# Kernel optimization log

Measured on AMD Instinct MI355X. Metric: run time of the kernel, lower is better.

## Reference

```python
import jax, jax.numpy as jnp
import numpy as np

# dims: T time steps, B batch, F clinical features, H GRU hidden, NH heads, DFF ffn dim, AH single-attn hidden
T, B, F, H, NH, DFF, AH = 128, 256, 76, 64, 4, 256, 8


def setup_inputs() -> dict:
    key = jax.random.key(0)
    ks = jax.random.split(key, 32)
    s = 0.1
    def u(k, shape):
        return jax.random.uniform(k, shape, jnp.float32, -s, s)
    return {
        "x": jax.random.normal(ks[0], (T, B, F), jnp.float32),
        # per-feature GRU(1, H) weight stacks (torch gate order: r, z, n)
        "gru_w_ih": u(ks[1], (F, 3 * H)),          # input dim is 1 -> squeezed
        "gru_w_hh": u(ks[2], (F, 3 * H, H)),
        "gru_b_ih": jnp.zeros((F, 3 * H), jnp.float32),
        "gru_b_hh": jnp.zeros((F, 3 * H), jnp.float32),
        # per-feature SingleAttention('new', time_aware) params
        "att_Wt": u(ks[3], (F, H, AH)),
        "att_Wx": u(ks[4], (F, H, AH)),
        "att_rate": jnp.full((F,), 0.8, jnp.float32),
        # multi-head self-attention over the feature axis
        "mha_wq": u(ks[5], (H, H)), "mha_bq": jnp.zeros((H,), jnp.float32),
        "mha_wk": u(ks[6], (H, H)), "mha_bk": jnp.zeros((H,), jnp.float32),
        "mha_wv": u(ks[7], (H, H)), "mha_bv": jnp.zeros((H,), jnp.float32),
        "mha_wo": u(ks[8], (H, H)), "mha_bo": jnp.zeros((H,), jnp.float32),
        # position-wise feed forward
        "ffn_w1": u(ks[9], (H, DFF)), "ffn_b1": jnp.zeros((DFF,), jnp.float32),
        "ffn_w2": u(ks[10], (DFF, H)), "ffn_b2": jnp.zeros((H,), jnp.float32),
        # FinalAttentionQKV ('mul')
        "fa_wq": u(ks[11], (H, H)), "fa_bq": jnp.zeros((H,), jnp.float32),
        "fa_wk": u(ks[12], (H, H)), "fa_bk": jnp.zeros((H,), jnp.float32),
        "fa_wv": u(ks[13], (H, H)), "fa_bv": jnp.zeros((H,), jnp.float32),
        # output head
        "out0_w": u(ks[14], (H, H)), "out0_b": jnp.zeros((H,), jnp.float32),
        "out1_w": u(ks[15], (H, 1)), "out1_b": jnp.zeros((1,), jnp.float32),
    }


def reference(x, gru_w_ih, gru_w_hh, gru_b_ih, gru_b_hh,
              att_Wt, att_Wx, att_rate,
              mha_wq, mha_bq, mha_wk, mha_bk, mha_wv, mha_bv, mha_wo, mha_bo,
              ffn_w1, ffn_b1, ffn_w2, ffn_b2,
              fa_wq, fa_bq, fa_wk, fa_bk, fa_wv, fa_bv,
              out0_w, out0_b, out1_w, out1_b):
    # x: (T, B, F); torch permutes to (B, T, F)
    Ts, Bsz, Fd = x.shape
    Hd = gru_w_hh.shape[-1]
    dk = Hd // NH

    # ---- all F GRU(1,H) channels fused into one scan (vectorized over F) ----
    xs = jnp.transpose(x, (0, 2, 1))  # (T, F, B)

    def step(h, x_t):  # h: (F,B,H), x_t: (F,B)
        gx = x_t[:, :, None] * gru_w_ih[:, None, :] + gru_b_ih[:, None, :]      # (F,B,3H)
        gh = jnp.einsum('fbh,fgh->fbg', h, gru_w_hh) + gru_b_hh[:, None, :]     # (F,B,3H)
        rx, zx, nx = jnp.split(gx, 3, axis=-1)
        rh, zh, nh = jnp.split(gh, 3, axis=-1)
        r = jax.nn.sigmoid(rx + rh)
        z = jax.nn.sigmoid(zx + zh)
        n = jnp.tanh(nx + r * nh)
        h_new = (1.0 - z) * n + z * h
        return h_new, h_new

    h0 = jnp.zeros((Fd, Bsz, Hd), x.dtype)
    _, hs = jax.lax.scan(step, h0, xs)        # (T, F, B, H)
    hs = jnp.transpose(hs, (1, 2, 0, 3))       # (F, B, T, H)

    # ---- per-feature SingleAttention, type='new', time-aware ----
    q = jnp.einsum('fbh,fha->fba', hs[:, :, -1, :], att_Wt)   # (F,B,AH)
    k = jnp.einsum('fbth,fha->fbta', hs, att_Wx)              # (F,B,T,AH)
    dp = jnp.einsum('fba,fbta->fbt', q, k)                    # (F,B,T)
    sig = jax.nn.sigmoid(dp)
    decay = jnp.arange(Ts, 0, -1, dtype=x.dtype)              # T..1 (time_decays + 1)
    denom = jax.nn.sigmoid(att_rate)[:, None, None] * (jnp.log(2.72 + (1.0 - sig)) * decay)
    e = jax.nn.relu(sig / denom)
    a = jax.nn.softmax(e, axis=-1)
    emb = jnp.einsum('fbt,fbth->bfh', a, hs)                  # (B, F, H)

    def lin(t, w, b):
        return t @ w + b

    # ---- multi-head self-attention over the F axis + residual ----
    # NOTE: original lambda ignores its (layernormed) argument, so LN is dead code.
    def heads(t):
        return t.reshape(Bsz, Fd, NH, dk).transpose(0, 2, 1, 3)
    qh = heads(lin(emb, mha_wq, mha_bq))
    kh = heads(lin(emb, mha_wk, mha_bk))
    vh = heads(lin(emb, mha_wv, mha_bv))
    scores = jnp.einsum('bhqd,bhkd->bhqk', qh, kh) / jnp.sqrt(jnp.asarray(dk, x.dtype))
    attn = jax.nn.softmax(scores, axis=-1)
    ctx = jnp.einsum('bhqk,bhkd->bhqd', attn, vh).transpose(0, 2, 1, 3).reshape(Bsz, Fd, Hd)
    ctx = emb + lin(ctx, mha_wo, mha_bo)

    # ---- position-wise feed-forward + residual ----
    ctx = ctx + lin(jax.nn.relu(lin(ctx, ffn_w1, ffn_b1)), ffn_w2, ffn_b2)

    # ---- FinalAttentionQKV, type='mul' ----
    fq = lin(ctx[:, -1, :], fa_wq, fa_bq)      # (B,H)
    fk = lin(ctx, fa_wk, fa_bk)                # (B,F,H)
    fv = lin(ctx, fa_wv, fa_bv)                # (B,F,H)
    fe = jnp.einsum('bfh,bh->bf', fk, fq)
    fa_w = jax.nn.softmax(fe, axis=1)
    v = jnp.einsum('bf,bfh->bh', fa_w, fv)     # (B,H)

    # ---- output head ----
    out = jax.nn.sigmoid(lin(jax.nn.relu(lin(v, out0_w, out0_b)), out1_w, out1_b))
    return out  # (B, 1)
```

## Files before the change

kernel.cpp:

```cpp
#include <hip/hip_runtime.h>
#include <hip/hip_bf16.h>
#include <cstdint>
#include <cstddef>

#define TT 128
#define BBATCH 256
#define FFEAT 76
#define HDIM 64
#define NHEAD 4
#define DKH 16
#define DFF1 256
#define AH1 8
#define NROWS (BBATCH * FFEAT)

#define LOG2E 1.4426950408889634f

typedef __attribute__((ext_vector_type(8))) short bf16x8;
typedef __attribute__((ext_vector_type(4))) float f32x4;

__device__ __forceinline__ float fast_sigmoid(float v) {
    float p = __builtin_amdgcn_exp2f(-v * LOG2E);
    return __builtin_amdgcn_rcpf(1.0f + p);
}
__device__ __forceinline__ float fast_tanh(float v) {
    float p = __builtin_amdgcn_exp2f(v * (2.0f * LOG2E));
    return 1.0f - 2.0f * __builtin_amdgcn_rcpf(1.0f + p);
}
__device__ __forceinline__ short f2bf(float x) {
    __hip_bfloat16 h = __float2bfloat16(x);
    return *reinterpret_cast<short*>(&h);
}
__device__ __forceinline__ float bf2f(unsigned short s) {
    return __uint_as_float(((unsigned)s) << 16);
}
__device__ __forceinline__ unsigned pack_bf16(float a, float b) {
    unsigned ua = (unsigned)(unsigned short)f2bf(a);
    unsigned ub = (unsigned)(unsigned short)f2bf(b);
    return ua | (ub << 16);
}

__global__ __launch_bounds__(64) void gru_scan_kernel(
    const float* __restrict__ x, const float* __restrict__ w_ih,
    const float* __restrict__ w_hh, const float* __restrict__ b_ih,
    const float* __restrict__ b_hh, const float* __restrict__ Wt,
    const float* __restrict__ Wx, int f_base,
    __hip_bfloat16* __restrict__ hs, float* __restrict__ wtil)
{
    const int f_loc = blockIdx.y;
    const int f     = f_base + f_loc;
    const int b0    = blockIdx.x * 16;
    const int lane  = threadIdx.x;
    const int c     = lane & 15;
    const int q     = lane >> 4;

    __shared__ float x_lds[TT][16];
    __shared__ float wt_s[64][8];
    __shared__ float wx_s[64][8];
    __shared__ short hx[16][72];
    __shared__ float q_s[16][8];

    for (int i = lane; i < TT * 16; i += 64) {
        int t = i >> 4, b = i & 15;
        x_lds[t][b] = x[((size_t)t * BBATCH + b0 + b) * FFEAT + f];
    }
    for (int i = lane; i < 512; i += 64) {
        ((float*)wt_s)[i] = Wt[(size_t)f * 512 + i];
        ((float*)wx_s)[i] = Wx[(size_t)f * 512 + i];
    }
    __syncthreads();

    bf16x8 afr[12][2];
    {
        const float* whh_f = w_hh + (size_t)f * 192 * 64;
        #pragma unroll
        for (int nt = 0; nt < 12; ++nt) {
            int gate = nt >> 2, tt = nt & 3;
            int urow = (c >> 2) * 8 + (tt & 1) * 4 + (c & 3) + (tt >> 1) * 32;
            const float* row = whh_f + (size_t)(gate * 64 + urow) * 64;
            #pragma unroll
            for (int kq = 0; kq < 2; ++kq) {
                bf16x8 fr;
                #pragma unroll
                for (int j = 0; j < 8; ++j) fr[j] = f2bf(row[kq * 32 + q * 8 + j]);
                afr[nt][kq] = fr;
            }
        }
    }
    float wr[4][4], wz[4][4], wn[4][4], bnx[4][4];
    f32x4 biasv[12];
    #pragma unroll
    for (int tt = 0; tt < 4; ++tt) {
        #pragma unroll
        for (int r = 0; r < 4; ++r) {
            int u = q * 8 + (tt & 1) * 4 + r + (tt >> 1) * 32;
            wr[tt][r]  = w_ih[f*192 + u];
            wz[tt][r]  = w_ih[f*192 + 64 + u];
            wn[tt][r]  = w_ih[f*192 + 128 + u];
            bnx[tt][r] = b_ih[f*192 + 128 + u];
            biasv[tt][r]     = b_ih[f*192 + u]      + b_hh[f*192 + u];
            biasv[4 + tt][r] = b_ih[f*192 + 64 + u] + b_hh[f*192 + 64 + u];
            biasv[8 + tt][r] = b_hh[f*192 + 128 + u];
        }
    }

    float hprev[4][4];
    #pragma unroll
    for (int tt = 0; tt < 4; ++tt)
        #pragma unroll
        for (int r = 0; r < 4; ++r) hprev[tt][r] = 0.f;

    bf16x8 hb0 = {0,0,0,0,0,0,0,0};
    bf16x8 hb1 = {0,0,0,0,0,0,0,0};

    short* hs_b = (short*)hs + ((size_t)f_loc * BBATCH + b0 + c) * TT * HDIM;

    for (int t = 0; t < TT; ++t) {
        f32x4 acc[12];
        #pragma unroll
        for (int nt = 0; nt < 12; ++nt) {
            f32x4 a = __builtin_amdgcn_mfma_f32_16x16x32_bf16(afr[nt][0], hb0, biasv[nt], 0, 0, 0);
            acc[nt]  = __builtin_amdgcn_mfma_f32_16x16x32_bf16(afr[nt][1], hb1, a, 0, 0, 0);
        }

        float xv = x_lds[t][c];
        float hn4[4][4];
        #pragma unroll
        for (int tt = 0; tt < 4; ++tt) {
            #pragma unroll
            for (int r = 0; r < 4; ++r) {
                float R  = fmaf(xv, wr[tt][r], acc[tt][r]);
                float Z  = fmaf(xv, wz[tt][r], acc[4 + tt][r]);
                float NX = fmaf(xv, wn[tt][r], bnx[tt][r]);
                float rg = fast_sigmoid(R);
                float zg = fast_sigmoid(Z);
                float ng = fast_tanh(fmaf(rg, acc[8 + tt][r], NX));
                float hn = fmaf(zg, hprev[tt][r] - ng, ng);
                hprev[tt][r] = hn;
                hn4[tt][r] = hn;
            }
        }
        {
            union { int4 i; bf16x8 v; } u0, u1;
            u0.i.x = pack_bf16(hn4[0][0], hn4[0][1]);
            u0.i.y = pack_bf16(hn4[0][2], hn4[0][3]);
            u0.i.z = pack_bf16(hn4[1][0], hn4[1][1]);
            u0.i.w = pack_bf16(hn4[1][2], hn4[1][3]);
            u1.i.x = pack_bf16(hn4[2][0], hn4[2][1]);
            u1.i.y = pack_bf16(hn4[2][2], hn4[2][3]);
            u1.i.z = pack_bf16(hn4[3][0], hn4[3][1]);
            u1.i.w = pack_bf16(hn4[3][2], hn4[3][3]);
            hb0 = u0.v; hb1 = u1.v;
        }
        short* dst = hs_b + (size_t)t * HDIM + q * 8;
        *(bf16x8*)dst = hb0;
        *(bf16x8*)(dst + 32) = hb1;
    }

    *(bf16x8*)&hx[c][q * 8]      = hb0;
    *(bf16x8*)&hx[c][32 + q * 8] = hb1;

    #pragma unroll
    for (int rr = 0; rr < 2; ++rr) {
        int role = rr * 64 + lane;
        int b = role >> 3, a = role & 7;
        float s = 0.f;
        #pragma unroll 8
        for (int j = 0; j < 64; ++j)
            s = fmaf(bf2f((unsigned short)hx[b][j]), wt_s[j][a], s);
        q_s[b][a] = s;
    }
    {
        int b = lane >> 2, jb = (lane & 3) * 16;
        float qreg[8];
        #pragma unroll
        for (int a = 0; a < 8; ++a) qreg[a] = q_s[b][a];
        float* wt_out = wtil + ((size_t)(b0 + b) * FFEAT + f) * HDIM + jb;
        #pragma unroll
        for (int j4 = 0; j4 < 4; ++j4) {
            float4 v;
            #pragma unroll
            for (int jj = 0; jj < 4; ++jj) {
                int j = jb + j4 * 4 + jj;
                float s = 0.f;
                #pragma unroll
                for (int a = 0; a < 8; ++a) s = fmaf(wx_s[j][a], qreg[a], s);
                (&v.x)[jj] = s;
            }
            *(float4*)&wt_out[j4 * 4] = v;
        }
    }
}

__global__ __launch_bounds__(256) void attn2_kernel(
    const __hip_bfloat16* __restrict__ hs, const float* __restrict__ wtil,
    const float* __restrict__ rate, int f_base, float* __restrict__ emb)
{
    const int w     = threadIdx.x >> 6;
    const int lane  = threadIdx.x & 63;
    const int b     = blockIdx.x * 4 + w;
    const int f_loc = blockIdx.y;
    const int f     = f_base + f_loc;
    const int g     = lane >> 3;
    const int i     = lane & 7;

    float wv[8];
    {
        const float4* src = (const float4*)(wtil + ((size_t)b * FFEAT + f) * HDIM + 8 * i);
        float4 a = src[0], c = src[1];
        wv[0]=a.x; wv[1]=a.y; wv[2]=a.z; wv[3]=a.w;
        wv[4]=c.x; wv[5]=c.y; wv[6]=c.z; wv[7]=c.w;
    }
    const float rs = fast_sigmoid(rate[f]);
    const uint4* basev = (const uint4*)((const short*)hs +
                          ((size_t)f_loc * BBATCH + b) * TT * HDIM);

    float m = -1.0e30f, s = 0.f;
    float o[8];
    #pragma unroll
    for (int j = 0; j < 8; ++j) o[j] = 0.f;

    #pragma unroll 4
    for (int it = 0; it < 16; ++it) {
        const int t = it * 8 + g;
        uint4 U = basev[t * 8 + i];
        float h[8];
        h[0] = __uint_as_float(U.x << 16); h[1] = __uint_as_float(U.x & 0xffff0000u);
        h[2] = __uint_as_float(U.y << 16); h[3] = __uint_as_float(U.y & 0xffff0000u);
        h[4] = __uint_as_float(U.z << 16); h[5] = __uint_as_float(U.z & 0xffff0000u);
        h[6] = __uint_as_float(U.w << 16); h[7] = __uint_as_float(U.w & 0xffff0000u);
        float dp = 0.f;
        #pragma unroll
        for (int j = 0; j < 8; ++j) dp = fmaf(h[j], wv[j], dp);
        dp += __shfl_xor(dp, 1, 64);
        dp += __shfl_xor(dp, 2, 64);
        dp += __shfl_xor(dp, 4, 64);
        float sig = fast_sigmoid(dp);
        float den = rs * (__logf(2.72f + (1.0f - sig)) * (float)(TT - t));
        float e = fmaxf(sig / den, 0.0f);
        float nm = fmaxf(m, e);
        float sc = __builtin_amdgcn_exp2f((m - nm) * LOG2E);
        float p  = __builtin_amdgcn_exp2f((e - nm) * LOG2E);
        s = fmaf(s, sc, p);
        #pragma unroll
        for (int j = 0; j < 8; ++j) o[j] = fmaf(o[j], sc, p * h[j]);
        m = nm;
    }
    #pragma unroll
    for (int k = 8; k <= 32; k <<= 1) {
        float om = __shfl_xor(m, k, 64);
        float os = __shfl_xor(s, k, 64);
        float nm = fmaxf(m, om);
        float sa = __builtin_amdgcn_exp2f((m - nm) * LOG2E);
        float sb = __builtin_amdgcn_exp2f((om - nm) * LOG2E);
        s = s * sa + os * sb;
        #pragma unroll
        for (int j = 0; j < 8; ++j) {
            float oo = __shfl_xor(o[j], k, 64);
            o[j] = o[j] * sa + oo * sb;
        }
        m = nm;
    }
    if (g == 0) {
        float inv = __builtin_amdgcn_rcpf(s);
        float4 v0, v1;
        v0.x = o[0]*inv; v0.y = o[1]*inv; v0.z = o[2]*inv; v0.w = o[3]*inv;
        v1.x = o[4]*inv; v1.y = o[5]*inv; v1.z = o[6]*inv; v1.w = o[7]*inv;
        float* dst = &emb[((size_t)b * FFEAT + f) * HDIM + 8 * i];
        *(float4*)dst       = v0;
        *(float4*)(dst + 4) = v1;
    }
}

struct GemmP {
    const float* X;
    const float* W[3];
    const float* B[3];
    const float* R;
    float* Y[3];
    int K;
    int Nfull;
    int act;
};

__global__ __launch_bounds__(256) void gemm_kernel(GemmP A)
{
    __shared__ float xs[64][65];
    __shared__ float ws[64][68];

    const int tid = threadIdx.x;
    const int tx  = tid & 15;
    const int ty  = tid >> 4;
    const int m0  = blockIdx.x * 64;
    const int n0  = blockIdx.y * 64;
    const int z   = blockIdx.z;

    const float* W = A.W[z];
    const float* Bv = A.B[z];
    float* Y = A.Y[z];
    const int K = A.K, Nfull = A.Nfull;

    float acc[4][4];
    #pragma unroll
// ... 192 lines not shown
{
    const float* x     = (const float*)d_in[0];
    const float* w_ih  = (const float*)d_in[1];
    const float* w_hh  = (const float*)d_in[2];
    const float* b_ih  = (const float*)d_in[3];
    const float* b_hh  = (const float*)d_in[4];
    const float* attWt = (const float*)d_in[5];
    const float* attWx = (const float*)d_in[6];
    const float* attRt = (const float*)d_in[7];
    const float* wq    = (const float*)d_in[8];
    const float* bq    = (const float*)d_in[9];
    const float* wk    = (const float*)d_in[10];
    const float* bk    = (const float*)d_in[11];
    const float* wv    = (const float*)d_in[12];
    const float* bv    = (const float*)d_in[13];
    const float* wo    = (const float*)d_in[14];
    const float* bo    = (const float*)d_in[15];
    const float* w1    = (const float*)d_in[16];
    const float* b1    = (const float*)d_in[17];
    const float* w2    = (const float*)d_in[18];
    const float* b2    = (const float*)d_in[19];
    const float* faq   = (const float*)d_in[20];
    const float* fabq  = (const float*)d_in[21];
    const float* fak   = (const float*)d_in[22];
    const float* fabk  = (const float*)d_in[23];
    const float* fav   = (const float*)d_in[24];
    const float* fabv  = (const float*)d_in[25];
    const float* o0w   = (const float*)d_in[26];
    const float* o0b   = (const float*)d_in[27];
    const float* o1w   = (const float*)d_in[28];
    const float* o1b   = (const float*)d_in[29];
    float* out = (float*)d_out;

    const size_t emb_bytes  = (size_t)NROWS * HDIM * 4;
    const size_t wtil_bytes = (size_t)NROWS * HDIM * 4;
    const size_t R64        = (size_t)NROWS * HDIM;
    const size_t tail_bytes = 12 * R64 * 4;

    const int chunk_opts[6] = {76, 38, 19, 4, 2, 1};
    int FC = 0;
    for (int i = 0; i < 6; ++i) {
        size_t hs_b = (size_t)chunk_opts[i] * BBATCH * TT * HDIM * 2;
        size_t scratch = hs_b > tail_bytes ? hs_b : tail_bytes;
        if (emb_bytes + wtil_bytes + scratch <= ws_size) { FC = chunk_opts[i]; break; }
    }
    if (FC == 0) {
        ws_report_kernel<<<dim3((out_size + 255) / 256), dim3(256), 0, stream>>>(
            out, out_size, (float)((double)ws_size / (1024.0 * 1024.0)));
        return;
    }

    float* emb  = (float*)d_ws;
    float* wtil = (float*)((char*)d_ws + emb_bytes);
    char*  scratch = (char*)d_ws + emb_bytes + wtil_bytes;
    __hip_bfloat16* hs = (__hip_bfloat16*)scratch;

    for (int f0 = 0; f0 < FFEAT; f0 += FC) {
        int fc = (FFEAT - f0 < FC) ? (FFEAT - f0) : FC;
        gru_scan_kernel<<<dim3(16, fc), dim3(64), 0, stream>>>(
            x, w_ih, w_hh, b_ih, b_hh, attWt, attWx, f0, hs, wtil);
        attn2_kernel<<<dim3(BBATCH / 4, fc), dim3(256), 0, stream>>>(
            hs, wtil, attRt, f0, emb);
    }

    float* ts   = (float*)scratch;
    float* q    = ts;
    float* k    = ts + 1*R64;
    float* v    = ts + 2*R64;
    float* ctx  = ts + 3*R64;
    float* ctx2 = ts + 4*R64;
    float* hid  = ts + 5*R64;
    float* ctx3 = ts + 9*R64;
    float* fk   = ts + 10*R64;
    float* fv   = ts + 11*R64;

    const int MB = NROWS / 64;

    {
        GemmP A = { emb, {wq, wk, wv}, {bq, bk, bv}, nullptr, {q, k, v}, 64, 64, 0 };
        gemm_kernel<<<dim3(MB, 1, 3), dim3(256), 0, stream>>>(A);
    }
    mha_core_kernel<<<dim3(BBATCH, NHEAD), dim3(256), 0, stream>>>(q, k, v, ctx);
    {
        GemmP A = { ctx, {wo, nullptr, nullptr}, {bo, nullptr, nullptr}, emb,
                    {ctx2, nullptr, nullptr}, 64, 64, 0 };
        gemm_kernel<<<dim3(MB, 1, 1), dim3(256), 0, stream>>>(A);
    }
    {
        GemmP A = { ctx2, {w1, nullptr, nullptr}, {b1, nullptr, nullptr}, nullptr,
                    {hid, nullptr, nullptr}, 64, 256, 1 };
        gemm_kernel<<<dim3(MB, 4, 1), dim3(256), 0, stream>>>(A);
    }
    {
        GemmP A = { hid, {w2, nullptr, nullptr}, {b2, nullptr, nullptr}, ctx2,
                    {ctx3, nullptr, nullptr}, 256, 64, 0 };
// ... 11 lines not shown
```

Measured before the change: 568.7 us.

## Split GRU hidden units across two waves with LDS double-buffered state exchange

After: 644.5 us. 13.3% more time.

```diff
diff --git a/kernel.cpp b/kernel.cpp
--- a/kernel.cpp
+++ b/kernel.cpp
@@ -39,7 +39,7 @@
     return ua | (ub << 16);
 }
 
-__global__ __launch_bounds__(64) void gru_scan_kernel(
+__global__ __launch_bounds__(128) void gru_scan_kernel(
     const float* __restrict__ x, const float* __restrict__ w_ih,
     const float* __restrict__ w_hh, const float* __restrict__ b_ih,
     const float* __restrict__ b_hh, const float* __restrict__ Wt,
@@ -49,138 +49,138 @@
     const int f_loc = blockIdx.y;
     const int f     = f_base + f_loc;
     const int b0    = blockIdx.x * 16;
-    const int lane  = threadIdx.x;
+    const int tid   = threadIdx.x;
+    const int w     = tid >> 6;
+    const int lane  = tid & 63;
     const int c     = lane & 15;
     const int q     = lane >> 4;
 
     __shared__ float x_lds[TT][16];
     __shared__ float wt_s[64][8];
     __shared__ float wx_s[64][8];
-    __shared__ short hx[16][72];
+    __shared__ short hbuf[2][16][72];
     __shared__ float q_s[16][8];
 
-    for (int i = lane; i < TT * 16; i += 64) {
+    for (int i = tid; i < TT * 16; i += 128) {
         int t = i >> 4, b = i & 15;
         x_lds[t][b] = x[((size_t)t * BBATCH + b0 + b) * FFEAT + f];
     }
-    for (int i = lane; i < 512; i += 64) {
+    for (int i = tid; i < 512; i += 128) {
         ((float*)wt_s)[i] = Wt[(size_t)f * 512 + i];
         ((float*)wx_s)[i] = Wx[(size_t)f * 512 + i];
     }
-    __syncthreads();
-
-    bf16x8 afr[12][2];
+    {
+        short* hz = (short*)hbuf;
+        for (int i = tid; i < 16 * 72; i += 128) hz[i] = 0;
+    }
+    __syncthreads();
+
+    bf16x8 afr[6][2];
     {
         const float* whh_f = w_hh + (size_t)f * 192 * 64;
         #pragma unroll
-        for (int nt = 0; nt < 12; ++nt) {
-            int gate = nt >> 2, tt = nt & 3;
-            int urow = (c >> 2) * 8 + (tt & 1) * 4 + (c & 3) + (tt >> 1) * 32;
-            const float* row = whh_f + (size_t)(gate * 64 + urow) * 64;
+        for (int nt = 0; nt < 6; ++nt) {
+            int g = nt >> 1, t2 = nt & 1;
+            const float* rp = whh_f + (size_t)(g * 64 + w * 32 + t2 * 16 + c) * 64;
             #pragma unroll
             for (int kq = 0; kq < 2; ++kq) {
                 bf16x8 fr;
                 #pragma unroll
-                for (int j = 0; j < 8; ++j) fr[j] = f2bf(row[kq * 32 + q * 8 + j]);
+                for (int j = 0; j < 8; ++j) fr[j] = f2bf(rp[kq * 32 + q * 8 + j]);
                 afr[nt][kq] = fr;
             }
         }
     }
-    float wr[4][4], wz[4][4], wn[4][4], bnx[4][4];
-    f32x4 biasv[12];
-    #pragma unroll
-    for (int tt = 0; tt < 4; ++tt) {
+    float wr[2][4], wz[2][4], wn[2][4], bnx[2][4];
+    f32x4 biasv[6];
+    #pragma unroll
+    for (int t2 = 0; t2 < 2; ++t2) {
         #pragma unroll
         for (int r = 0; r < 4; ++r) {
-            int u = q * 8 + (tt & 1) * 4 + r + (tt >> 1) * 32;
-            wr[tt][r]  = w_ih[f*192 + u];
-            wz[tt][r]  = w_ih[f*192 + 64 + u];
-            wn[tt][r]  = w_ih[f*192 + 128 + u];
-            bnx[tt][r] = b_ih[f*192 + 128 + u];
-            biasv[tt][r]     = b_ih[f*192 + u]      + b_hh[f*192 + u];
-            biasv[4 + tt][r] = b_ih[f*192 + 64 + u] + b_hh[f*192 + 64 + u];
-            biasv[8 + tt][r] = b_hh[f*192 + 128 + u];
-        }
-    }
-
-    float hprev[4][4];
-    #pragma unroll
-    for (int tt = 0; tt < 4; ++tt)
-        #pragma unroll
-        for (int r = 0; r < 4; ++r) hprev[tt][r] = 0.f;
-
-    bf16x8 hb0 = {0,0,0,0,0,0,0,0};
-    bf16x8 hb1 = {0,0,0,0,0,0,0,0};
-
+            int u = w * 32 + t2 * 16 + q * 4 + r;
+            wr[t2][r]  = w_ih[f*192 + u];
+            wz[t2][r]  = w_ih[f*192 + 64 + u];
+            wn[t2][r]  = w_ih[f*192 + 128 + u];
+            bnx[t2][r] = b_ih[f*192 + 128 + u];
+            biasv[t2][r]     = b_ih[f*192 + u]      + b_hh[f*192 + u];
+            biasv[2 + t2][r] = b_ih[f*192 + 64 + u] + b_hh[f*192 + 64 + u];
+            biasv[4 + t2][r] = b_hh[f*192 + 128 + u];
+        }
+    }
+
+    float hprev[2][4];
+    #pragma unroll
+    for (int t2 = 0; t2 < 2; ++t2)
+        #pragma unroll
+        for (int r = 0; r < 4; ++r) hprev[t2][r] = 0.f;
+
+    int cur = 0;
     short* hs_b = (short*)hs + ((size_t)f_loc * BBATCH + b0 + c) * TT * HDIM;
 
     for (int t = 0; t < TT; ++t) {
-        f32x4 acc[12];
-        #pragma unroll
-        for (int nt = 0; nt < 12; ++nt) {
+        bf16x8 hb0 = *(bf16x8*)&hbuf[cur][c][q * 8];
+        bf16x8 hb1 = *(bf16x8*)&hbuf[cur][c][32 + q * 8];
+
+        f32x4 acc[6];
+        #pragma unroll
+        for (int nt = 0; nt < 6; ++nt) {
             f32x4 a = __builtin_amdgcn_mfma_f32_16x16x32_bf16(afr[nt][0], hb0, biasv[nt], 0, 0, 0);
             acc[nt]  = __builtin_amdgcn_mfma_f32_16x16x32_bf16(afr[nt][1], hb1, a, 0, 0, 0);
         }
 
         float xv = x_lds[t][c];
-        float hn4[4][4];
-        #pragma unroll
-        for (int tt = 0; tt < 4; ++tt) {
+        float hn4[2][4];
+        #pragma unroll
+        for (int t2 = 0; t2 < 2; ++t2) {
             #pragma unroll
             for (int r = 0; r < 4; ++r) {
-                float R  = fmaf(xv, wr[tt][r], acc[tt][r]);
-                float Z  = fmaf(xv, wz[tt][r], acc[4 + tt][r]);
-                float NX = fmaf(xv, wn[tt][r], bnx[tt][r]);
+                float R  = fmaf(xv, wr[t2][r], acc[t2][r]);
+                float Z  = fmaf(xv, wz[t2][r], acc[2 + t2][r]);
+                float NX = fmaf(xv, wn[t2][r], bnx[t2][r]);
                 float rg = fast_sigmoid(R);
                 float zg = fast_sigmoid(Z);
-                float ng = fast_tanh(fmaf(rg, acc[8 + tt][r], NX));
-                float hn = fmaf(zg, hprev[tt][r] - ng, ng);
-                hprev[tt][r] = hn;
-                hn4[tt][r] = hn;
+                float ng = fast_tanh(fmaf(rg, acc[4 + t2][r], NX));
+                float hn = fmaf(zg, hprev[t2][r] - ng, ng);
+                hprev[t2][r] = hn;
+                hn4[t2][r] = hn;
             }
         }
-        {
-            union { int4 i; bf16x8 v; } u0, u1;
-            u0.i.x = pack_bf16(hn4[0][0], hn4[0][1]);
-            u0.i.y = pack_bf16(hn4[0][2], hn4[0][3]);
-            u0.i.z = pack_bf16(hn4[1][0], hn4[1][1]);
-            u0.i.w = pack_bf16(hn4[1][2], hn4[1][3]);
-            u1.i.x = pack_bf16(hn4[2][0], hn4[2][1]);
-            u1.i.y = pack_bf16(hn4[2][2], hn4[2][3]);
-            u1.i.z = pack_bf16(hn4[3][0], hn4[3][1]);
-            u1.i.w = pack_bf16(hn4[3][2], hn4[3][3]);
-            hb0 = u0.v; hb1 = u1.v;
-        }
-        short* dst = hs_b + (size_t)t * HDIM + q * 8;
-        *(bf16x8*)dst = hb0;
-        *(bf16x8*)(dst + 32) = hb1;
-    }
-
-    *(bf16x8*)&hx[c][q * 8]      = hb0;
-    *(bf16x8*)&hx[c][32 + q * 8] = hb1;
-
-    #pragma unroll
-    for (int rr = 0; rr < 2; ++rr) {
-        int role = rr * 64 + lane;
-        int b = role >> 3, a = role & 7;
+        uint2 pk0, pk1;
+        pk0.x = pack_bf16(hn4[0][0], hn4[0][1]);
+        pk0.y = pack_bf16(hn4[0][2], hn4[0][3]);
+        pk1.x = pack_bf16(hn4[1][0], hn4[1][1]);
+        pk1.y = pack_bf16(hn4[1][2], hn4[1][3]);
+        short* hd = &hbuf[cur ^ 1][c][w * 32 + q * 4];
+        *(uint2*)hd        = pk0;
+        *(uint2*)(hd + 16) = pk1;
+        short* gd = hs_b + (size_t)t * HDIM + w * 32 + q * 4;
+        *(uint2*)gd        = pk0;
+        *(uint2*)(gd + 16) = pk1;
+        __syncthreads();
+        cur ^= 1;
+    }
+
+    {
+        int b = tid >> 3, a = tid & 7;
         float s = 0.f;
         #pragma unroll 8
         for (int j = 0; j < 64; ++j)
-            s = fmaf(bf2f((unsigned short)hx[b][j]), wt_s[j][a], s);
+            s = fmaf(bf2f((unsigned short)hbuf[cur][b][j]), wt_s[j][a], s);
         q_s[b][a] = s;
     }
-    {
-        int b = lane >> 2, jb = (lane & 3) * 16;
+    __syncthreads();
+    {
+        int b = tid >> 3, seg = tid & 7;
         float qreg[8];
         #pragma unroll
         for (int a = 0; a < 8; ++a) qreg[a] = q_s[b][a];
-        float* wt_out = wtil + ((size_t)(b0 + b) * FFEAT + f) * HDIM + jb;
-        #pragma unroll
-        for (int j4 = 0; j4 < 4; ++j4) {
+        float* wt_out = wtil + ((size_t)(b0 + b) * FFEAT + f) * HDIM + seg * 8;
+        #pragma unroll
+        for (int j4 = 0; j4 < 2; ++j4) {
             float4 v;
             #pragma unroll
             for (int jj = 0; jj < 4; ++jj) {
-                int j = jb + j4 * 4 + jj;
+                int j = seg * 8 + j4 * 4 + jj;
                 float s = 0.f;
                 #pragma unroll
                 for (int a = 0; a < 8; ++a) s = fmaf(wx_s[j][a], qreg[a], s);
@@ -206,9 +206,9 @@
     float wv[8];
     {
         const float4* src = (const float4*)(wtil + ((size_t)b * FFEAT + f) * HDIM + 8 * i);
-        float4 a = src[0], c = src[1];
+        float4 a = src[0], c2 = src[1];
         wv[0]=a.x; wv[1]=a.y; wv[2]=a.z; wv[3]=a.w;
-        wv[4]=c.x; wv[5]=c.y; wv[6]=c.z; wv[7]=c.w;
+        wv[4]=c2.x; wv[5]=c2.y; wv[6]=c2.z; wv[7]=c2.w;
     }
     const float rs = fast_sigmoid(rate[f]);
     const uint4* basev = (const uint4*)((const short*)hs +
@@ -551,7 +551,7 @@
 
     for (int f0 = 0; f0 < FFEAT; f0 += FC) {
         int fc = (FFEAT - f0 < FC) ? (FFEAT - f0) : FC;
-        gru_scan_kernel<<<dim3(16, fc), dim3(64), 0, stream>>>(
+        gru_scan_kernel<<<dim3(16, fc), dim3(128), 0, stream>>>(
             x, w_ih, w_hh, b_ih, b_hh, attWt, attWx, f0, hs, wtil);
         attn2_kernel<<<dim3(BBATCH / 4, fc), dim3(256), 0, stream>>>(
             hs, wtil, attRt, f0, emb);
```

## Fuse GRU scan and time attention into one pipelined launch with double-buffered states

Applied to the files above, without the earlier changes.

New measurement: 819.2 us. +44.1%, slower.

```diff
diff --git a/kernel.cpp b/kernel.cpp
--- a/kernel.cpp
+++ b/kernel.cpp
@@ -12,6 +12,7 @@
 #define DFF1 256
 #define AH1 8
 #define NROWS (BBATCH * FFEAT)
+#define FC 19
 
 #define LOG2E 1.4426950408889634f
 
@@ -39,235 +40,235 @@
     return ua | (ub << 16);
 }
 
-__global__ __launch_bounds__(64) void gru_scan_kernel(
+__global__ __launch_bounds__(64) void fused_scan_attn_kernel(
     const float* __restrict__ x, const float* __restrict__ w_ih,
     const float* __restrict__ w_hh, const float* __restrict__ b_ih,
     const float* __restrict__ b_hh, const float* __restrict__ Wt,
-    const float* __restrict__ Wx, int f_base,
-    __hip_bfloat16* __restrict__ hs, float* __restrict__ wtil)
+    const float* __restrict__ Wx, const float* __restrict__ rate,
+    int ngru, int f0_gru, __hip_bfloat16* __restrict__ hs_w,
+    int f0_att, const __hip_bfloat16* __restrict__ hs_r,
+    float* __restrict__ wtil, float* __restrict__ emb)
 {
-    const int f_loc = blockIdx.y;
-    const int f     = f_base + f_loc;
-    const int b0    = blockIdx.x * 16;
-    const int lane  = threadIdx.x;
-    const int c     = lane & 15;
-    const int q     = lane >> 4;
-
     __shared__ float x_lds[TT][16];
     __shared__ float wt_s[64][8];
     __shared__ float wx_s[64][8];
     __shared__ short hx[16][72];
     __shared__ float q_s[16][8];
 
-    for (int i = lane; i < TT * 16; i += 64) {
-        int t = i >> 4, b = i & 15;
-        x_lds[t][b] = x[((size_t)t * BBATCH + b0 + b) * FFEAT + f];
-    }
-    for (int i = lane; i < 512; i += 64) {
-        ((float*)wt_s)[i] = Wt[(size_t)f * 512 + i];
-        ((float*)wx_s)[i] = Wx[(size_t)f * 512 + i];
-    }
-    __syncthreads();
-
-    bf16x8 afr[12][2];
-    {
-        const float* whh_f = w_hh + (size_t)f * 192 * 64;
-        #pragma unroll
-        for (int nt = 0; nt < 12; ++nt) {
-            int gate = nt >> 2, tt = nt & 3;
-            int urow = (c >> 2) * 8 + (tt & 1) * 4 + (c & 3) + (tt >> 1) * 32;
-            const float* row = whh_f + (size_t)(gate * 64 + urow) * 64;
-            #pragma unroll
-            for (int kq = 0; kq < 2; ++kq) {
-                bf16x8 fr;
+    const int gid  = blockIdx.x;
+    const int lane = threadIdx.x;
+
+    if (gid < ngru) {
+        const int f_loc = gid >> 4;
+        const int f     = f0_gru + f_loc;
+        const int b0    = (gid & 15) * 16;
+        const int c     = lane & 15;
+        const int q     = lane >> 4;
+
+        for (int i = lane; i < TT * 16; i += 64) {
+            int t = i >> 4, b = i & 15;
+            x_lds[t][b] = x[((size_t)t * BBATCH + b0 + b) * FFEAT + f];
+        }
+        for (int i = lane; i < 512; i += 64) {
+            ((float*)wt_s)[i] = Wt[(size_t)f * 512 + i];
+            ((float*)wx_s)[i] = Wx[(size_t)f * 512 + i];
+        }
+        __syncthreads();
+
+        bf16x8 afr[12][2];
+        {
+            const float* whh_f = w_hh + (size_t)f * 192 * 64;
+            #pragma unroll
+            for (int nt = 0; nt < 12; ++nt) {
+                int gate = nt >> 2, tt = nt & 3;
+                int urow = (c >> 2) * 8 + (tt & 1) * 4 + (c & 3) + (tt >> 1) * 32;
+                const float* row = whh_f + (size_t)(gate * 64 + urow) * 64;
                 #pragma unroll
-                for (int j = 0; j < 8; ++j) fr[j] = f2bf(row[kq * 32 + q * 8 + j]);
-                afr[nt][kq] = fr;
-            }
-        }
-    }
-    float wr[4][4], wz[4][4], wn[4][4], bnx[4][4];
-    f32x4 biasv[12];
-    #pragma unroll
-    for (int tt = 0; tt < 4; ++tt) {
-        #pragma unroll
-        for (int r = 0; r < 4; ++r) {
-            int u = q * 8 + (tt & 1) * 4 + r + (tt >> 1) * 32;
-            wr[tt][r]  = w_ih[f*192 + u];
-            wz[tt][r]  = w_ih[f*192 + 64 + u];
-            wn[tt][r]  = w_ih[f*192 + 128 + u];
-            bnx[tt][r] = b_ih[f*192 + 128 + u];
-            biasv[tt][r]     = b_ih[f*192 + u]      + b_hh[f*192 + u];
-            biasv[4 + tt][r] = b_ih[f*192 + 64 + u] + b_hh[f*192 + 64 + u];
-            biasv[8 + tt][r] = b_hh[f*192 + 128 + u];
-        }
-    }
-
-    float hprev[4][4];
-    #pragma unroll
-    for (int tt = 0; tt < 4; ++tt)
-        #pragma unroll
-        for (int r = 0; r < 4; ++r) hprev[tt][r] = 0.f;
-
-    bf16x8 hb0 = {0,0,0,0,0,0,0,0};
-    bf16x8 hb1 = {0,0,0,0,0,0,0,0};
-
-    short* hs_b = (short*)hs + ((size_t)f_loc * BBATCH + b0 + c) * TT * HDIM;
-
-    for (int t = 0; t < TT; ++t) {
-        f32x4 acc[12];
-        #pragma unroll
-        for (int nt = 0; nt < 12; ++nt) {
-            f32x4 a = __builtin_amdgcn_mfma_f32_16x16x32_bf16(afr[nt][0], hb0, biasv[nt], 0, 0, 0);
-            acc[nt]  = __builtin_amdgcn_mfma_f32_16x16x32_bf16(afr[nt][1], hb1, a, 0, 0, 0);
-        }
-
-        float xv = x_lds[t][c];
-        float hn4[4][4];
+                for (int kq = 0; kq < 2; ++kq) {
+                    bf16x8 fr;
+                    #pragma unroll
+                    for (int j = 0; j < 8; ++j) fr[j] = f2bf(row[kq * 32 + q * 8 + j]);
+                    afr[nt][kq] = fr;
+                }
+            }
+        }
+        float wr[4][4], wz[4][4], wn[4][4], bnx[4][4];
+        f32x4 biasv[12];
         #pragma unroll
         for (int tt = 0; tt < 4; ++tt) {
             #pragma unroll
             for (int r = 0; r < 4; ++r) {
-                float R  = fmaf(xv, wr[tt][r], acc[tt][r]);
-                float Z  = fmaf(xv, wz[tt][r], acc[4 + tt][r]);
-                float NX = fmaf(xv, wn[tt][r], bnx[tt][r]);
-                float rg = fast_sigmoid(R);
-                float zg = fast_sigmoid(Z);
-                float ng = fast_tanh(fmaf(rg, acc[8 + tt][r], NX));
-                float hn = fmaf(zg, hprev[tt][r] - ng, ng);
-                hprev[tt][r] = hn;
-                hn4[tt][r] = hn;
-            }
+                int u = q * 8 + (tt & 1) * 4 + r + (tt >> 1) * 32;
+                wr[tt][r]  = w_ih[f*192 + u];
+                wz[tt][r]  = w_ih[f*192 + 64 + u];
+                wn[tt][r]  = w_ih[f*192 + 128 + u];
+                bnx[tt][r] = b_ih[f*192 + 128 + u];
+                biasv[tt][r]     = b_ih[f*192 + u]      + b_hh[f*192 + u];
+                biasv[4 + tt][r] = b_ih[f*192 + 64 + u] + b_hh[f*192 + 64 + u];
+                biasv[8 + tt][r] = b_hh[f*192 + 128 + u];
+            }
+        }
+
+        float hprev[4][4];
+        #pragma unroll
+        for (int tt = 0; tt < 4; ++tt)
+            #pragma unroll
+            for (int r = 0; r < 4; ++r) hprev[tt][r] = 0.f;
+
+        bf16x8 hb0 = {0,0,0,0,0,0,0,0};
+        bf16x8 hb1 = {0,0,0,0,0,0,0,0};
+
+        short* hs_b = (short*)hs_w + ((size_t)f_loc * BBATCH + b0 + c) * TT * HDIM;
+
+        for (int t = 0; t < TT; ++t) {
+            f32x4 acc[12];
+            #pragma unroll
+            for (int nt = 0; nt < 12; ++nt) {
+                f32x4 a = __builtin_amdgcn_mfma_f32_16x16x32_bf16(afr[nt][0], hb0, biasv[nt], 0, 0, 0);
+                acc[nt]  = __builtin_amdgcn_mfma_f32_16x16x32_bf16(afr[nt][1], hb1, a, 0, 0, 0);
+            }
+
+            float xv = x_lds[t][c];
+            float hn4[4][4];
+            #pragma unroll
+            for (int tt = 0; tt < 4; ++tt) {
+                #pragma unroll
+                for (int r = 0; r < 4; ++r) {
+                    float R  = fmaf(xv, wr[tt][r], acc[tt][r]);
+                    float Z  = fmaf(xv, wz[tt][r], acc[4 + tt][r]);
+                    float NX = fmaf(xv, wn[tt][r], bnx[tt][r]);
+                    float rg = fast_sigmoid(R);
+                    float zg = fast_sigmoid(Z);
+                    float ng = fast_tanh(fmaf(rg, acc[8 + tt][r], NX));
+                    float hn = fmaf(zg, hprev[tt][r] - ng, ng);
+                    hprev[tt][r] = hn;
+                    hn4[tt][r] = hn;
+                }
+            }
+            {
+                union { int4 i; bf16x8 v; } u0, u1;
+                u0.i.x = pack_bf16(hn4[0][0], hn4[0][1]);
+                u0.i.y = pack_bf16(hn4[0][2], hn4[0][3]);
+                u0.i.z = pack_bf16(hn4[1][0], hn4[1][1]);
+                u0.i.w = pack_bf16(hn4[1][2], hn4[1][3]);
+                u1.i.x = pack_bf16(hn4[2][0], hn4[2][1]);
+                u1.i.y = pack_bf16(hn4[2][2], hn4[2][3]);
+                u1.i.z = pack_bf16(hn4[3][0], hn4[3][1]);
+                u1.i.w = pack_bf16(hn4[3][2], hn4[3][3]);
+                hb0 = u0.v; hb1 = u1.v;
+            }
+            short* dst = hs_b + (size_t)t * HDIM + q * 8;
+            *(bf16x8*)dst = hb0;
+            *(bf16x8*)(dst + 32) = hb1;
+        }
+
+        *(bf16x8*)&hx[c][q * 8]      = hb0;
+        *(bf16x8*)&hx[c][32 + q * 8] = hb1;
+
+        #pragma unroll
+        for (int rr = 0; rr < 2; ++rr) {
+            int role = rr * 64 + lane;
+            int b = role >> 3, a = role & 7;
+            float s = 0.f;
+            #pragma unroll 8
+            for (int j = 0; j < 64; ++j)
+                s = fmaf(bf2f((unsigned short)hx[b][j]), wt_s[j][a], s);
+            q_s[b][a] = s;
         }
         {
-            union { int4 i; bf16x8 v; } u0, u1;
-            u0.i.x = pack_bf16(hn4[0][0], hn4[0][1]);
-            u0.i.y = pack_bf16(hn4[0][2], hn4[0][3]);
-            u0.i.z = pack_bf16(hn4[1][0], hn4[1][1]);
-            u0.i.w = pack_bf16(hn4[1][2], hn4[1][3]);
-            u1.i.x = pack_bf16(hn4[2][0], hn4[2][1]);
-            u1.i.y = pack_bf16(hn4[2][2], hn4[2][3]);
-            u1.i.z = pack_bf16(hn4[3][0], hn4[3][1]);
-            u1.i.w = pack_bf16(hn4[3][2], hn4[3][3]);
-            hb0 = u0.v; hb1 = u1.v;
-        }
-        short* dst = hs_b + (size_t)t * HDIM + q * 8;
-        *(bf16x8*)dst = hb0;
-        *(bf16x8*)(dst + 32) = hb1;
-    }
-
-    *(bf16x8*)&hx[c][q * 8]      = hb0;
-    *(bf16x8*)&hx[c][32 + q * 8] = hb1;
-
-    #pragma unroll
-    for (int rr = 0; rr < 2; ++rr) {
-        int role = rr * 64 + lane;
-        int b = role >> 3, a = role & 7;
-        float s = 0.f;
-        #pragma unroll 8
-        for (int j = 0; j < 64; ++j)
-            s = fmaf(bf2f((unsigned short)hx[b][j]), wt_s[j][a], s);
-        q_s[b][a] = s;
-    }
-    {
-        int b = lane >> 2, jb = (lane & 3) * 16;
-        float qreg[8];
-        #pragma unroll
-        for (int a = 0; a < 8; ++a) qreg[a] = q_s[b][a];
-        float* wt_out = wtil + ((size_t)(b0 + b) * FFEAT + f) * HDIM + jb;
-        #pragma unroll
-        for (int j4 = 0; j4 < 4; ++j4) {
-            float4 v;
-            #pragma unroll
-            for (int jj = 0; jj < 4; ++jj) {
-                int j = jb + j4 * 4 + jj;
-                float s = 0.f;
+            int b = lane >> 2, jb = (lane & 3) * 16;
+            float qreg[8];
+            #pragma unroll
+            for (int a = 0; a < 8; ++a) qreg[a] = q_s[b][a];
+            float* wt_out = wtil + ((size_t)(b0 + b) * FFEAT + f) * HDIM + jb;
+            #pragma unroll
+            for (int j4 = 0; j4 < 4; ++j4) {
+                float4 v;
                 #pragma unroll
-                for (int a = 0; a < 8; ++a) s = fmaf(wx_s[j][a], qreg[a], s);
-                (&v.x)[jj] = s;
-            }
-            *(float4*)&wt_out[j4 * 4] = v;
-        }
-    }
-}
-
-__global__ __launch_bounds__(256) void attn2_kernel(
-    const __hip_bfloat16* __restrict__ hs, const float* __restrict__ wtil,
-    const float* __restrict__ rate, int f_base, float* __restrict__ emb)
-{
-    const int w     = threadIdx.x >> 6;
-    const int lane  = threadIdx.x & 63;
-    const int b     = blockIdx.x * 4 + w;
-    const int f_loc = blockIdx.y;
-    const int f     = f_base + f_loc;
-    const int g     = lane >> 3;
-    const int i     = lane & 7;
-
-    float wv[8];
-    {
-        const float4* src = (const float4*)(wtil + ((size_t)b * FFEAT + f) * HDIM + 8 * i);
-        float4 a = src[0], c = src[1];
-        wv[0]=a.x; wv[1]=a.y; wv[2]=a.z; wv[3]=a.w;
-        wv[4]=c.x; wv[5]=c.y; wv[6]=c.z; wv[7]=c.w;
-    }
-    const float rs = fast_sigmoid(rate[f]);
-    const uint4* basev = (const uint4*)((const short*)hs +
-                          ((size_t)f_loc * BBATCH + b) * TT * HDIM);
-
-    float m = -1.0e30f, s = 0.f;
-    float o[8];
-    #pragma unroll
-    for (int j = 0; j < 8; ++j) o[j] = 0.f;
-
-    #pragma unroll 4
-    for (int it = 0; it < 16; ++it) {
-        const int t = it * 8 + g;
-        uint4 U = basev[t * 8 + i];
-        float h[8];
-        h[0] = __uint_as_float(U.x << 16); h[1] = __uint_as_float(U.x & 0xffff0000u);
-        h[2] = __uint_as_float(U.y << 16); h[3] = __uint_as_float(U.y & 0xffff0000u);
-        h[4] = __uint_as_float(U.z << 16); h[5] = __uint_as_float(U.z & 0xffff0000u);
-        h[6] = __uint_as_float(U.w << 16); h[7] = __uint_as_float(U.w & 0xffff0000u);
-        float dp = 0.f;
-        #pragma unroll
-        for (int j = 0; j < 8; ++j) dp = fmaf(h[j], wv[j], dp);
-        dp += __shfl_xor(dp, 1, 64);
-        dp += __shfl_xor(dp, 2, 64);
-        dp += __shfl_xor(dp, 4, 64);
-        float sig = fast_sigmoid(dp);
-        float den = rs * (__logf(2.72f + (1.0f - sig)) * (float)(TT - t));
-        float e = fmaxf(sig / den, 0.0f);
-        float nm = fmaxf(m, e);
-        float sc = __builtin_amdgcn_exp2f((m - nm) * LOG2E);
-        float p  = __builtin_amdgcn_exp2f((e - nm) * LOG2E);
-        s = fmaf(s, sc, p);
-        #pragma unroll
-        for (int j = 0; j < 8; ++j) o[j] = fmaf(o[j], sc, p * h[j]);
-        m = nm;
-    }
-    #pragma unroll
-    for (int k = 8; k <= 32; k <<= 1) {
-        float om = __shfl_xor(m, k, 64);
-        float os = __shfl_xor(s, k, 64);
-        float nm = fmaxf(m, om);
-        float sa = __builtin_amdgcn_exp2f((m - nm) * LOG2E);
-        float sb = __builtin_amdgcn_exp2f((om - nm) * LOG2E);
-        s = s * sa + os * sb;
-        #pragma unroll
-        for (int j = 0; j < 8; ++j) {
-            float oo = __shfl_xor(o[j], k, 64);
-            o[j] = o[j] * sa + oo * sb;
-        }
-        m = nm;
-    }
-    if (g == 0) {
-        float inv = __builtin_amdgcn_rcpf(s);
-        float4 v0, v1;
-        v0.x = o[0]*inv; v0.y = o[1]*inv; v0.z = o[2]*inv; v0.w = o[3]*inv;
-        v1.x = o[4]*inv; v1.y = o[5]*inv; v1.z = o[6]*inv; v1.w = o[7]*inv;
-        float* dst = &emb[((size_t)b * FFEAT + f) * HDIM + 8 * i];
-        *(float4*)dst       = v0;
-        *(float4*)(dst + 4) = v1;
+                for (int jj = 0; jj < 4; ++jj) {
+                    int j = jb + j4 * 4 + jj;
+                    float s = 0.f;
+                    #pragma unroll
+                    for (int a = 0; a < 8; ++a) s = fmaf(wx_s[j][a], qreg[a], s);
+                    (&v.x)[jj] = s;
+                }
+                *(float4*)&wt_out[j4 * 4] = v;
+            }
+        }
+    } else {
+        const int aid   = gid - ngru;
+        const int b     = aid & 255;
+        const int f_loc = aid >> 8;
+        const int f     = f0_att + f_loc;
+        const int g     = lane >> 3;
+        const int i     = lane & 7;
+
+        float wv[8];
+        {
+            const float4* src = (const float4*)(wtil + ((size_t)b * FFEAT + f) * HDIM + 8 * i);
+            float4 a = src[0], c2 = src[1];
+            wv[0]=a.x; wv[1]=a.y; wv[2]=a.z; wv[3]=a.w;
+            wv[4]=c2.x; wv[5]=c2.y; wv[6]=c2.z; wv[7]=c2.w;
+        }
+        const float rs = fast_sigmoid(rate[f]);
+        const uint4* basev = (const uint4*)((const short*)hs_r +
+                              ((size_t)f_loc * BBATCH + b) * TT * HDIM);
+
+        float m = -1.0e30f, s = 0.f;
+        float o[8];
+        #pragma unroll
+        for (int j = 0; j < 8; ++j) o[j] = 0.f;
+
+        #pragma unroll 4
+        for (int it = 0; it < 16; ++it) {
+            const int t = it * 8 + g;
+            uint4 U = basev[t * 8 + i];
+            float h[8];
+            h[0] = __uint_as_float(U.x << 16); h[1] = __uint_as_float(U.x & 0xffff0000u);
+            h[2] = __uint_as_float(U.y << 16); h[3] = __uint_as_float(U.y & 0xffff0000u);
+            h[4] = __uint_as_float(U.z << 16); h[5] = __uint_as_float(U.z & 0xffff0000u);
+            h[6] = __uint_as_float(U.w << 16); h[7] = __uint_as_float(U.w & 0xffff0000u);
+            float dp = 0.f;
+            #pragma unroll
+            for (int j = 0; j < 8; ++j) dp = fmaf(h[j], wv[j], dp);
+            dp += __shfl_xor(dp, 1, 64);
+            dp += __shfl_xor(dp, 2, 64);
+            dp += __shfl_xor(dp, 4, 64);
+            float sig = fast_sigmoid(dp);
+            float den = rs * (__logf(2.72f + (1.0f - sig)) * (float)(TT - t));
+            float e = fmaxf(sig / den, 0.0f);
+            float nm = fmaxf(m, e);
+            float sc = __builtin_amdgcn_exp2f((m - nm) * LOG2E);
+            float p  = __builtin_amdgcn_exp2f((e - nm) * LOG2E);
+            s = fmaf(s, sc, p);
+            #pragma unroll
+            for (int j = 0; j < 8; ++j) o[j] = fmaf(o[j], sc, p * h[j]);
+            m = nm;
+        }
+        #pragma unroll
+        for (int k = 8; k <= 32; k <<= 1) {
+            float om = __shfl_xor(m, k, 64);
+            float os = __shfl_xor(s, k, 64);
+            float nm = fmaxf(m, om);
+            float sa = __builtin_amdgcn_exp2f((m - nm) * LOG2E);
+            float sb = __builtin_amdgcn_exp2f((om - nm) * LOG2E);
+            s = s * sa + os * sb;
+            #pragma unroll
+            for (int j = 0; j < 8; ++j) {
+                float oo = __shfl_xor(o[j], k, 64);
+                o[j] = o[j] * sa + oo * sb;
+            }
+            m = nm;
+        }
+        if (g == 0) {
+            float inv = __builtin_amdgcn_rcpf(s);
+            float4 v0, v1;
+            v0.x = o[0]*inv; v0.y = o[1]*inv; v0.z = o[2]*inv; v0.w = o[3]*inv;
+            v1.x = o[4]*inv; v1.y = o[5]*inv; v1.z = o[6]*inv; v1.w = o[7]*inv;
+            float* dst = &emb[((size_t)b * FFEAT + f) * HDIM + 8 * i];
+            *(float4*)dst       = v0;
+            *(float4*)(dst + 4) = v1;
+        }
     }
 }
 
@@ -528,17 +529,13 @@
 
     const size_t emb_bytes  = (size_t)NROWS * HDIM * 4;
     const size_t wtil_bytes = (size_t)NROWS * HDIM * 4;
+    const size_t hs_half    = (size_t)FC * BBATCH * TT * HDIM * 2;
     const size_t R64        = (size_t)NROWS * HDIM;
     const size_t tail_bytes = 12 * R64 * 4;
-
-    const int chunk_opts[6] = {76, 38, 19, 4, 2, 1};
-    int FC = 0;
-    for (int i = 0; i < 6; ++i) {
-        size_t hs_b = (size_t)chunk_opts[i] * BBATCH * TT * HDIM * 2;
-        size_t scratch = hs_b > tail_bytes ? hs_b : tail_bytes;
-        if (emb_bytes + wtil_bytes + scratch <= ws_size) { FC = chunk_opts[i]; break; }
-    }
-    if (FC == 0) {
+    const size_t scratch_sz = (2 * hs_half > tail_bytes) ? 2 * hs_half : tail_bytes;
+    const size_t need = emb_bytes + wtil_bytes + scratch_sz;
+
+    if (need > ws_size) {
         ws_report_kernel<<<dim3((out_size + 255) / 256), dim3(256), 0, stream>>>(
             out, out_size, (float)((double)ws_size / (1024.0 * 1024.0)));
         return;
@@ -547,14 +544,22 @@
     float* emb  = (float*)d_ws;
     float* wtil = (float*)((char*)d_ws + emb_bytes);
     char*  scratch = (char*)d_ws + emb_bytes + wtil_bytes;
-    __hip_bfloat16* hs = (__hip_bfloat16*)scratch;
-
-    for (int f0 = 0; f0 < FFEAT; f0 += FC) {
-        int fc = (FFEAT - f0 < FC) ? (FFEAT - f0) : FC;
-        gru_scan_kernel<<<dim3(16, fc), dim3(64), 0, stream>>>(
-            x, w_ih, w_hh, b_ih, b_hh, attWt, attWx, f0, hs, wtil);
-        attn2_kernel<<<dim3(BBATCH / 4, fc), dim3(256), 0, stream>>>(
-            hs, wtil, attRt, f0, emb);
+    __hip_bfloat16* hs[2] = {
+        (__hip_bfloat16*)scratch,
+        (__hip_bfloat16*)(scratch + hs_half)
+    };
+
+    const int NCHUNK = FFEAT / FC;
+    for (int c = 0; c <= NCHUNK; ++c) {
+        const int gru_on = (c < NCHUNK);
+        const int att_on = (c > 0);
+        const int ngru = gru_on ? 16 * FC : 0;
+        const int natt = att_on ? BBATCH * FC : 0;
+        fused_scan_attn_kernel<<<dim3(ngru + natt), dim3(64), 0, stream>>>(
+            x, w_ih, w_hh, b_ih, b_hh, attWt, attWx, attRt,
+            ngru, c * FC, hs[c & 1],
+            (c - 1) * FC, hs[(c - 1) & 1],
+            wtil, emb);
     }
 
     float* ts   = (float*)scratch;
```

## Fuse time-aware attention into GRU scan kernel and drop wtil buffer

Applied to the files above, without the earlier changes.

New measurement: 639.0 us. 1.12x slower.

```diff
diff --git a/kernel.cpp b/kernel.cpp
--- a/kernel.cpp
+++ b/kernel.cpp
@@ -39,12 +39,12 @@
     return ua | (ub << 16);
 }
 
-__global__ __launch_bounds__(64) void gru_scan_kernel(
+__global__ __launch_bounds__(64) void gru_attn_kernel(
     const float* __restrict__ x, const float* __restrict__ w_ih,
     const float* __restrict__ w_hh, const float* __restrict__ b_ih,
     const float* __restrict__ b_hh, const float* __restrict__ Wt,
-    const float* __restrict__ Wx, int f_base,
-    __hip_bfloat16* __restrict__ hs, float* __restrict__ wtil)
+    const float* __restrict__ Wx, const float* __restrict__ rate,
+    int f_base, __hip_bfloat16* __restrict__ hs, float* __restrict__ emb)
 {
     const int f_loc = blockIdx.y;
     const int f     = f_base + f_loc;
@@ -58,6 +58,7 @@
     __shared__ float wx_s[64][8];
     __shared__ short hx[16][72];
     __shared__ float q_s[16][8];
+    __shared__ float wt_til[16][68];
 
     for (int i = lane; i < TT * 16; i += 64) {
         int t = i >> 4, b = i & 15;
@@ -174,7 +175,6 @@
         float qreg[8];
         #pragma unroll
         for (int a = 0; a < 8; ++a) qreg[a] = q_s[b][a];
-        float* wt_out = wtil + ((size_t)(b0 + b) * FFEAT + f) * HDIM + jb;
         #pragma unroll
         for (int j4 = 0; j4 < 4; ++j4) {
             float4 v;
@@ -186,88 +186,81 @@
                 for (int a = 0; a < 8; ++a) s = fmaf(wx_s[j][a], qreg[a], s);
                 (&v.x)[jj] = s;
             }
-            *(float4*)&wt_out[j4 * 4] = v;
-        }
-    }
-}
-
-__global__ __launch_bounds__(256) void attn2_kernel(
-    const __hip_bfloat16* __restrict__ hs, const float* __restrict__ wtil,
-    const float* __restrict__ rate, int f_base, float* __restrict__ emb)
-{
-    const int w     = threadIdx.x >> 6;
-    const int lane  = threadIdx.x & 63;
-    const int b     = blockIdx.x * 4 + w;
-    const int f_loc = blockIdx.y;
-    const int f     = f_base + f_loc;
-    const int g     = lane >> 3;
-    const int i     = lane & 7;
-
-    float wv[8];
-    {
-        const float4* src = (const float4*)(wtil + ((size_t)b * FFEAT + f) * HDIM + 8 * i);
-        float4 a = src[0], c = src[1];
-        wv[0]=a.x; wv[1]=a.y; wv[2]=a.z; wv[3]=a.w;
-        wv[4]=c.x; wv[5]=c.y; wv[6]=c.z; wv[7]=c.w;
-    }
+            *(float4*)&wt_til[b][jb + j4 * 4] = v;
+        }
+    }
+    __syncthreads();
+
     const float rs = fast_sigmoid(rate[f]);
-    const uint4* basev = (const uint4*)((const short*)hs +
-                          ((size_t)f_loc * BBATCH + b) * TT * HDIM);
-
-    float m = -1.0e30f, s = 0.f;
-    float o[8];
-    #pragma unroll
-    for (int j = 0; j < 8; ++j) o[j] = 0.f;
-
-    #pragma unroll 4
-    for (int it = 0; it < 16; ++it) {
-        const int t = it * 8 + g;
-        uint4 U = basev[t * 8 + i];
-        float h[8];
-        h[0] = __uint_as_float(U.x << 16); h[1] = __uint_as_float(U.x & 0xffff0000u);
-        h[2] = __uint_as_float(U.y << 16); h[3] = __uint_as_float(U.y & 0xffff0000u);
-        h[4] = __uint_as_float(U.z << 16); h[5] = __uint_as_float(U.z & 0xffff0000u);
-        h[6] = __uint_as_float(U.w << 16); h[7] = __uint_as_float(U.w & 0xffff0000u);
-        float dp = 0.f;
-        #pragma unroll
-        for (int j = 0; j < 8; ++j) dp = fmaf(h[j], wv[j], dp);
-        dp += __shfl_xor(dp, 1, 64);
-        dp += __shfl_xor(dp, 2, 64);
-        dp += __shfl_xor(dp, 4, 64);
-        float sig = fast_sigmoid(dp);
-        float den = rs * (__logf(2.72f + (1.0f - sig)) * (float)(TT - t));
-        float e = fmaxf(sig / den, 0.0f);
-        float nm = fmaxf(m, e);
-        float sc = __builtin_amdgcn_exp2f((m - nm) * LOG2E);
-        float p  = __builtin_amdgcn_exp2f((e - nm) * LOG2E);
-        s = fmaf(s, sc, p);
-        #pragma unroll
-        for (int j = 0; j < 8; ++j) o[j] = fmaf(o[j], sc, p * h[j]);
-        m = nm;
-    }
-    #pragma unroll
-    for (int k = 8; k <= 32; k <<= 1) {
-        float om = __shfl_xor(m, k, 64);
-        float os = __shfl_xor(s, k, 64);
-        float nm = fmaxf(m, om);
-        float sa = __builtin_amdgcn_exp2f((m - nm) * LOG2E);
-        float sb = __builtin_amdgcn_exp2f((om - nm) * LOG2E);
-        s = s * sa + os * sb;
-        #pragma unroll
-        for (int j = 0; j < 8; ++j) {
-            float oo = __shfl_xor(o[j], k, 64);
-            o[j] = o[j] * sa + oo * sb;
-        }
-        m = nm;
-    }
-    if (g == 0) {
-        float inv = __builtin_amdgcn_rcpf(s);
-        float4 v0, v1;
-        v0.x = o[0]*inv; v0.y = o[1]*inv; v0.z = o[2]*inv; v0.w = o[3]*inv;
-        v1.x = o[4]*inv; v1.y = o[5]*inv; v1.z = o[6]*inv; v1.w = o[7]*inv;
-        float* dst = &emb[((size_t)b * FFEAT + f) * HDIM + 8 * i];
-        *(float4*)dst       = v0;
-        *(float4*)(dst + 4) = v1;
+    const int g  = lane >> 3;
+    const int ii = lane & 7;
+
+    for (int bb = 0; bb < 16; ++bb) {
+        float wv[8];
+        {
+            float4 a = *(const float4*)&wt_til[bb][8 * ii];
+            float4 c2 = *(const float4*)&wt_til[bb][8 * ii + 4];
+            wv[0]=a.x; wv[1]=a.y; wv[2]=a.z; wv[3]=a.w;
+            wv[4]=c2.x; wv[5]=c2.y; wv[6]=c2.z; wv[7]=c2.w;
+        }
+        const uint4* basev = (const uint4*)((const short*)hs +
+                              ((size_t)f_loc * BBATCH + b0 + bb) * TT * HDIM);
+
+        float m = -1.0e30f, s = 0.f;
+        float o[8];
+        #pragma unroll
+        for (int j = 0; j < 8; ++j) o[j] = 0.f;
+
+        #pragma unroll 4
+        for (int it = 0; it < 16; ++it) {
+            const int t = it * 8 + g;
+            uint4 U = basev[t * 8 + ii];
+            float h[8];
+            h[0] = __uint_as_float(U.x << 16); h[1] = __uint_as_float(U.x & 0xffff0000u);
+            h[2] = __uint_as_float(U.y << 16); h[3] = __uint_as_float(U.y & 0xffff0000u);
+            h[4] = __uint_as_float(U.z << 16); h[5] = __uint_as_float(U.z & 0xffff0000u);
+            h[6] = __uint_as_float(U.w << 16); h[7] = __uint_as_float(U.w & 0xffff0000u);
+            float dp = 0.f;
+            #pragma unroll
+            for (int j = 0; j < 8; ++j) dp = fmaf(h[j], wv[j], dp);
+            dp += __shfl_xor(dp, 1, 64);
+            dp += __shfl_xor(dp, 2, 64);
+            dp += __shfl_xor(dp, 4, 64);
+            float sig = fast_sigmoid(dp);
+            float den = rs * (__logf(2.72f + (1.0f - sig)) * (float)(TT - t));
+            float e = fmaxf(sig / den, 0.0f);
+            float nm = fmaxf(m, e);
+            float sc = __builtin_amdgcn_exp2f((m - nm) * LOG2E);
+            float p  = __builtin_amdgcn_exp2f((e - nm) * LOG2E);
+            s = fmaf(s, sc, p);
+            #pragma unroll
+            for (int j = 0; j < 8; ++j) o[j] = fmaf(o[j], sc, p * h[j]);
+            m = nm;
+        }
+        #pragma unroll
+        for (int k = 8; k <= 32; k <<= 1) {
+            float om = __shfl_xor(m, k, 64);
+            float os = __shfl_xor(s, k, 64);
+            float nm = fmaxf(m, om);
+            float sa = __builtin_amdgcn_exp2f((m - nm) * LOG2E);
+            float sb = __builtin_amdgcn_exp2f((om - nm) * LOG2E);
+            s = s * sa + os * sb;
+            #pragma unroll
+            for (int j = 0; j < 8; ++j) {
+                float oo = __shfl_xor(o[j], k, 64);
+                o[j] = o[j] * sa + oo * sb;
+            }
+            m = nm;
+        }
+        if (g == 0) {
+            float inv = __builtin_amdgcn_rcpf(s);
+            float4 v0, v1;
+            v0.x = o[0]*inv; v0.y = o[1]*inv; v0.z = o[2]*inv; v0.w = o[3]*inv;
+            v1.x = o[4]*inv; v1.y = o[5]*inv; v1.z = o[6]*inv; v1.w = o[7]*inv;
+            float* dst = &emb[((size_t)(b0 + bb) * FFEAT + f) * HDIM + 8 * ii];
+            *(float4*)dst       = v0;
+            *(float4*)(dst + 4) = v1;
+        }
     }
 }
 
@@ -526,17 +519,16 @@
     const float* o1b   = (const float*)d_in[29];
     float* out = (float*)d_out;
 
-    const size_t emb_bytes  = (size_t)NROWS * HDIM * 4;
-    const size_t wtil_bytes = (size_t)NROWS * HDIM * 4;
-    const size_t R64        = (size_t)NROWS * HDIM;
+    const size_t emb_bytes = (size_t)NROWS * HDIM * 4;
+    const size_t R64       = (size_t)NROWS * HDIM;
     const size_t tail_bytes = 12 * R64 * 4;
 
-    const int chunk_opts[6] = {76, 38, 19, 4, 2, 1};
+    const int chunk_opts[5] = {38, 19, 4, 2, 1};
     int FC = 0;
-    for (int i = 0; i < 6; ++i) {
+    for (int i = 0; i < 5; ++i) {
         size_t hs_b = (size_t)chunk_opts[i] * BBATCH * TT * HDIM * 2;
         size_t scratch = hs_b > tail_bytes ? hs_b : tail_bytes;
-        if (emb_bytes + wtil_bytes + scratch <= ws_size) { FC = chunk_opts[i]; break; }
+        if (emb_bytes + scratch <= ws_size) { FC = chunk_opts[i]; break; }
     }
     if (FC == 0) {
         ws_report_kernel<<<dim3((out_size + 255) / 256), dim3(256), 0, stream>>>(
@@ -545,16 +537,13 @@
     }
 
     float* emb  = (float*)d_ws;
-    float* wtil = (float*)((char*)d_ws + emb_bytes);
-    char*  scratch = (char*)d_ws + emb_bytes + wtil_bytes;
+    char*  scratch = (char*)d_ws + emb_bytes;
     __hip_bfloat16* hs = (__hip_bfloat16*)scratch;
 
     for (int f0 = 0; f0 < FFEAT; f0 += FC) {
         int fc = (FFEAT - f0 < FC) ? (FFEAT - f0) : FC;
-        gru_scan_kernel<<<dim3(16, fc), dim3(64), 0, stream>>>(
-            x, w_ih, w_hh, b_ih, b_hh, attWt, attWx, f0, hs, wtil);
-        attn2_kernel<<<dim3(BBATCH / 4, fc), dim3(256), 0, stream>>>(
-            hs, wtil, attRt, f0, emb);
+        gru_attn_kernel<<<dim3(16, fc), dim3(64), 0, stream>>>(
+            x, w_ih, w_hh, b_ih, b_hh, attWt, attWx, attRt, f0, hs, emb);
     }
 
     float* ts   = (float*)scratch;
```
